# Kernel optimization log

Measured on AMD Instinct MI355X. Metric: run time of the kernel, lower is better.

The kernel has to match this reference:

```python
import jax, jax.numpy as jnp
import numpy as np

B, D, H, E, K = 16384, 1024, 256, 8, 2
EPS = 1e-9


def setup_inputs() -> dict:
    key = jax.random.key(0)
    ks = jax.random.split(key, 4)
    scale_in = 1.0 / np.sqrt(D)
    scale_h = 1.0 / np.sqrt(H)
    return {
        "x": jax.random.normal(ks[0], (B, D), dtype=jnp.float32),
        "gate_w": jax.random.normal(ks[1], (D, E), dtype=jnp.float32) * scale_in,
        "gate_b": jnp.zeros((E,), dtype=jnp.float32),
        "w1": jax.random.normal(ks[2], (E, D, H), dtype=jnp.float32) * scale_in,
        "b1": jnp.zeros((E, H), dtype=jnp.float32),
        "w2": jax.random.normal(ks[3], (E, H, D), dtype=jnp.float32) * scale_h,
        "b2": jnp.zeros((E, D), dtype=jnp.float32),
    }


def reference(x, gate_w, gate_b, w1, b1, w2, b2):
    # Gating: logits -> softmax -> top-k mask -> renormalize (top_k_gating)
    logits = x @ gate_w + gate_b                      # [B, E]
    probs = jax.nn.softmax(logits, axis=-1)           # [B, E]
    _, topk_idx = jax.lax.top_k(probs, K)             # [B, K]
    rows = jnp.arange(probs.shape[0])[:, None]
    mask = jnp.zeros_like(probs).at[rows, topk_idx].set(1.0)
    masked = probs * mask
    denom = jnp.clip(jnp.sum(masked, axis=-1, keepdims=True), EPS, None)
    gating_weights = masked / denom                   # [B, E]

    # Dense all-experts MLP: Linear -> GELU(exact) -> Linear, batched over E
    h = jax.nn.gelu(jnp.einsum('bd,edh->beh', x, w1) + b1, approximate=False)  # [B, E, H]
    expert_outs = jnp.einsum('beh,ehd->bed', h, w2) + b2                        # [B, E, D]

    # Gating-weighted sum over experts
    output = jnp.einsum('bed,be->bd', expert_outs, gating_weights)              # [B, D]
    return output
```

## Files before the change

kernel.cpp:

```cpp
#include <hip/hip_runtime.h>
#include <stdint.h>

#define BN 16384
#define DD 1024
#define HH 256
#define EE 8
#define GB 512
#define GR 32

typedef __attribute__((ext_vector_type(8))) short short8;
typedef __attribute__((ext_vector_type(4))) float floatx4;

__device__ __forceinline__ unsigned short f2bf(float f) {
  union { float f; unsigned int i; } v; v.f = f;
  unsigned int x = v.i;
  x += 0x7fffu + ((x >> 16) & 1u);
  return (unsigned short)(x >> 16);
}
__device__ __forceinline__ unsigned int pack2(float a, float b) {
  return (unsigned int)f2bf(a) | ((unsigned int)f2bf(b) << 16);
}
__device__ __forceinline__ float bf2f(unsigned int u16) {
  union { unsigned int i; float f; } v; v.i = u16 << 16; return v.f;
}
__device__ __forceinline__ void async16(const unsigned short* g, unsigned short* l) {
  __builtin_amdgcn_global_load_lds(
      (const __attribute__((address_space(1))) void*)g,
      (__attribute__((address_space(3))) void*)l, 16, 0, 0);
}

__global__ __launch_bounds__(256) void gating_kernel(
    const float* __restrict__ x,
    const float* __restrict__ gate_w,
    const float* __restrict__ gate_b,
    int* __restrict__ rinfo_e, float* __restrict__ rinfo_w,
    int* __restrict__ bhist,
    unsigned short* __restrict__ xb) {
  __shared__ int hist[EE];
  int tid = threadIdx.x;
  if (tid < EE) hist[tid] = 0;
  __syncthreads();
  int lane = tid & 63, wv = tid >> 6;
#pragma unroll 1
  for (int it = 0; it < GR / 4; it++) {
    int row = blockIdx.x * GR + it * 4 + wv;
    const float4* xr4 = (const float4*)(x + (size_t)row * DD);
    float acc[EE];
#pragma unroll
    for (int e = 0; e < EE; e++) acc[e] = 0.f;
#pragma unroll
    for (int i = 0; i < 4; i++) {
      int d4 = lane + i * 64;
      float4 xv = xr4[d4];
      if (xb) {
        uint2 st; st.x = pack2(xv.x, xv.y); st.y = pack2(xv.z, xv.w);
        *(uint2*)(xb + (size_t)row * DD + (size_t)d4 * 4) = st;
      }
      const float4* gp = (const float4*)gate_w + (size_t)d4 * 8;
      float xs[4] = {xv.x, xv.y, xv.z, xv.w};
#pragma unroll
      for (int j = 0; j < 4; j++) {
        float4 glo = gp[2 * j], ghi = gp[2 * j + 1];
        acc[0] += xs[j] * glo.x; acc[1] += xs[j] * glo.y;
        acc[2] += xs[j] * glo.z; acc[3] += xs[j] * glo.w;
        acc[4] += xs[j] * ghi.x; acc[5] += xs[j] * ghi.y;
        acc[6] += xs[j] * ghi.z; acc[7] += xs[j] * ghi.w;
      }
    }
#pragma unroll
    for (int s = 1; s < 64; s <<= 1) {
#pragma unroll
      for (int e = 0; e < EE; e++) acc[e] += __shfl_xor(acc[e], s, 64);
    }
    if (lane == 0) {
      float lg[EE];
#pragma unroll
      for (int e = 0; e < EE; e++) lg[e] = acc[e] + gate_b[e];
      int i1 = 0;
      for (int e = 1; e < EE; e++) if (lg[e] > lg[i1]) i1 = e;
      int i2 = (i1 == 0) ? 1 : 0;
      for (int e = 0; e < EE; e++) if (e != i1 && lg[e] > lg[i2]) i2 = e;
      float wA = 1.f / (1.f + __expf(lg[i2] - lg[i1]));
      float wB = 1.f - wA;
      rinfo_e[row] = i1 | (i2 << 8);
      rinfo_w[row * 2 + 0] = wA;
      rinfo_w[row * 2 + 1] = wB;
      atomicAdd(&hist[i1], 1);
      atomicAdd(&hist[i2], 1);
    }
  }
  __syncthreads();
  if (tid < EE) bhist[blockIdx.x * EE + tid] = hist[tid];
}

__global__ __launch_bounds__(256) void scan_kernel(
    const int* __restrict__ bhist, int* __restrict__ cnt, int* __restrict__ bbase) {
  __shared__ int cs[32][EE];
  __shared__ int ofs[EE];
  int tid = threadIdx.x;
  int g = tid & 7, c = tid >> 3;
  int s = 0;
#pragma unroll 1
  for (int b = c * 16; b < c * 16 + 16; b++) s += bhist[b * EE + g];
  cs[c][g] = s;
  __syncthreads();
  if (tid == 0) {
    int run = 0;
    for (int gg = 0; gg < EE; gg++) {
      int tot = 0;
      for (int cc = 0; cc < 32; cc++) tot += cs[cc][gg];
      cnt[gg] = tot;
      cnt[32 + gg] = run;
      ofs[gg] = run;
      run += tot;
    }
  }
  __syncthreads();
  if (tid < EE) {
    int run = ofs[tid];
#pragma unroll 1
    for (int cc = 0; cc < 32; cc++) { int t = cs[cc][tid]; cs[cc][tid] = run; run += t; }
  }
  __syncthreads();
  int run = cs[c][g];
#pragma unroll 1
  for (int b = c * 16; b < c * 16 + 16; b++) {
    bbase[b * EE + g] = run;
    run += bhist[b * EE + g];
  }
}

__global__ __launch_bounds__(64) void scatter_kernel(
    const int* __restrict__ rinfo_e, const float* rinfo_w,
    const int* __restrict__ bbase,
    int* __restrict__ rowidx, float* __restrict__ wgt, int* posmap) {
  __shared__ int curs[EE];
  int tid = threadIdx.x;
  if (tid < EE) curs[tid] = bbase[blockIdx.x * EE + tid];
  __syncthreads();
  if (tid < GR) {
    int row = blockIdx.x * GR + tid;
    int ee = rinfo_e[row];
    int e0 = ee & 255, e1 = (ee >> 8) & 255;
    float w0 = rinfo_w[row * 2 + 0];
    float w1 = rinfo_w[row * 2 + 1];
    int p0 = atomicAdd(&curs[e0], 1);
    rowidx[p0] = row; wgt[p0] = w0;
    int p1 = atomicAdd(&curs[e1], 1);
    rowidx[p1] = row; wgt[p1] = w1;
    posmap[row * 2 + 0] = p0;
    posmap[row * 2 + 1] = p1;
  }
}

__global__ void transpose_kernel(const float* __restrict__ src,
                                 unsigned short* __restrict__ dst, int R, int C) {
  __shared__ float tbuf[32][33];
  int e = blockIdx.z;
  int c0 = blockIdx.x * 32, r0 = blockIdx.y * 32;
  int tx = threadIdx.x, ty = threadIdx.y;
  const float* s = src + (size_t)e * R * C;
  unsigned short* d = dst + (size_t)e * R * C;
  for (int yy = ty; yy < 32; yy += 8)
    tbuf[yy][tx] = s[(size_t)(r0 + yy) * C + c0 + tx];
  __syncthreads();
  for (int yy = ty; yy < 32; yy += 8)
    d[(size_t)(c0 + yy) * R + r0 + tx] = f2bf(tbuf[tx][yy]);
}

template <bool ASYNC_A>
__global__ __launch_bounds__(256) void gemm1_kernel(
    const unsigned short* __restrict__ xb,
    const float* __restrict__ x,
    const unsigned short* __restrict__ w1t,
    const float* __restrict__ b1,
    const int* __restrict__ cnt,
    const int* __restrict__ rowidx,
    unsigned short* __restrict__ hbuf,
    int g0, int g1) {
  __shared__ unsigned short As[2][8192];
  __shared__ unsigned short Bs[2][8192];
  int t = blockIdx.x, g = -1, lt = 0;
#pragma unroll 1
  for (int gg = g0; gg < g1; gg++) {
    int nt = (cnt[gg] + 127) >> 7;
    if (t < nt) { g = gg; lt = t; break; }
    t -= nt;
  }
  if (g < 0) return;
  const int* offs = cnt + 32;
  int hb = offs[g0];
  int m0 = offs[g] + lt * 128;
  int mEnd = offs[g] + cnt[g];
  int e = g;
  int n0 = blockIdx.y * 128;
  const unsigned short* Bsrc = w1t + (size_t)e * HH * DD + (size_t)n0 * DD;
  int tid = threadIdx.x, lane = tid & 63, wv = tid >> 6;
  int wr = (wv >> 1) * 64, wc = (wv & 1) * 64;
  int lm = lane & 15, q = lane >> 4;
  int lm7 = lm & 7;
  floatx4 acc[4][4];
  floatx4 zero = {0.f, 0.f, 0.f, 0.f};
#pragma unroll
  for (int i = 0; i < 4; i++)
#pragma unroll
    for (int j = 0; j < 4; j++) acc[i][j] = zero;
  int srow = tid >> 3;
  int ssrc = (((tid & 7) ^ (srow & 7))) * 8;
  int sdst = (tid & 7) * 8;
  const unsigned short* gA[4];
  const float* gAf[4];
  const unsigned short* gBp[4];
#pragma unroll
  for (int i = 0; i < 4; i++) {
    int pos = m0 + i * 32 + srow;
    int grow = rowidx[pos < mEnd ? pos : m0];
    if (ASYNC_A) gA[i] = xb + (size_t)grow * DD + ssrc;
    else         gAf[i] = x + (size_t)grow * DD + ssrc;
    gBp[i] = Bsrc + (size_t)(i * 32 + srow) * DD + ssrc;
  }
  auto stageAsync = [&](int bufi) {
#pragma unroll
    for (int i = 0; i < 4; i++) async16(gA[i], &As[bufi][wv * 512 + i * 2048]);
#pragma unroll
    for (int i = 0; i < 4; i++) gA[i] += 64;
#pragma unroll
    for (int i = 0; i < 4; i++) async16(gBp[i], &Bs[bufi][wv * 512 + i * 2048]);
#pragma unroll
    for (int i = 0; i < 4; i++) gBp[i] += 64;
  };
  auto compute = [&](int bufi) {
#pragma unroll
    for (int ks = 0; ks < 2; ks++) {
      short8 a[4], b[4];
#pragma unroll
      for (int i = 0; i < 4; i++)
        a[i] = *(const short8*)&As[bufi][(wr + i * 16 + lm) * 64 + ((ks * 4 + q) ^ lm7) * 8];
#pragma unroll
      for (int j = 0; j < 4; j++)
        b[j] = *(const short8*)&Bs[bufi][(wc + j * 16 + lm) * 64 + ((ks * 4 + q) ^ lm7) * 8];
#pragma unroll
      for (int i = 0; i < 4; i++)
#pragma unroll
        for (int j = 0; j < 4; j++)
          acc[i][j] = __builtin_amdgcn_mfma_f32_16x16x32_bf16(b[j], a[i], acc[i][j], 0, 0, 0);
    }
  };
  if (ASYNC_A) {
    stageAsync(0);
    __syncthreads();
    int buf = 0;
#pragma unroll 1
    for (int tt = 0; tt < DD / 64; ++tt) {
      if (tt < DD / 64 - 1) stageAsync(buf ^ 1);
      compute(buf);
      __syncthreads();
      buf ^= 1;
    }
  } else {
#pragma unroll 1
    for (int k0 = 0; k0 < DD; k0 += 64) {
#pragma unroll
      for (int i = 0; i < 4; i++) {
        float4 f0 = *(const float4*)gAf[i];
        float4 f1 = *(const float4*)(gAf[i] + 4);
        gAf[i] += 64;
        uint4 av;
        av.x = pack2(f0.x, f0.y); av.y = pack2(f0.z, f0.w);
        av.z = pack2(f1.x, f1.y); av.w = pack2(f1.z, f1.w);
        *(uint4*)&As[0][(i * 32 + srow) * 64 + sdst] = av;
      }
#pragma unroll
      for (int i = 0; i < 4; i++) async16(gBp[i], &Bs[0][wv * 512 + i * 2048]);
#pragma unroll
      for (int i = 0; i < 4; i++) gBp[i] += 64;
      __syncthreads();
      compute(0);
      __syncthreads();
    }
  }
#pragma unroll
  for (int i = 0; i < 4; i++) {
    int pos = m0 + wr + i * 16 + lm;
    if (pos < mEnd) {
#pragma unroll
      for (int j = 0; j < 4; j++) {
        int col = n0 + wc + j * 16 + q * 4;
        const float4 bb = *(const float4*)(b1 + e * HH + col);
        float v0 = acc[i][j][0] + bb.x;
        float v1 = acc[i][j][1] + bb.y;
        float v2 = acc[i][j][2] + bb.z;
        float v3 = acc[i][j][3] + bb.w;
        v0 = 0.5f * v0 * (1.f + erff(v0 * 0.70710678118654752f));
        v1 = 0.5f * v1 * (1.f + erff(v1 * 0.70710678118654752f));
        v2 = 0.5f * v2 * (1.f + erff(v2 * 0.70710678118654752f));
        v3 = 0.5f * v3 * (1.f + erff(v3 * 0.70710678118654752f));
        uint2 st; st.x = pack2(v0, v1); st.y = pack2(v2, v3);
        *(uint2*)(hbuf + (size_t)(pos - hb) * HH + col) = st;
      }
    }
  }
}

template <bool EO>
__global__ __launch_bounds__(256) void gemm2_kernel(
    const unsigned short* __restrict__ hbuf,
    const unsigned short* __restrict__ w2t,
    const float* __restrict__ b2,
    const int* __restrict__ cnt,
    const int* __restrict__ rowidx,
    const float* __restrict__ wgt,
    unsigned short* __restrict__ eo,
    float* out,
    int g0, int g1) {
  __shared__ unsigned short As[128 * 64];
  __shared__ unsigned short Bs[128 * 64];
  int t = blockIdx.x, g = -1, lt = 0;
#pragma unroll 1
  for (int gg = g0; gg < g1; gg++) {
    int nt = (cnt[gg] + 127) >> 7;
    if (t < nt) { g = gg; lt = t; break; }
    t -= nt;
  }
  if (g < 0) return;
  const int* offs = cnt + 32;
  int hb = offs[g0];
  int m0 = offs[g] + lt * 128;
  int mEnd = offs[g] + cnt[g];
  int e = g;
  int n0 = blockIdx.y * 128;
  const unsigned short* Bsrc = w2t + (size_t)e * DD * HH + (size_t)n0 * HH;
  int tid = threadIdx.x, lane = tid & 63, wv = tid >> 6;
  int wr = (wv >> 1) * 64, wc = (wv & 1) * 64;
  int lm = lane & 15, q = lane >> 4;
  int lm7 = lm & 7;
  floatx4 acc[4][4];
  floatx4 zero = {0.f, 0.f, 0.f, 0.f};
#pragma unroll
  for (int i = 0; i < 4; i++)
#pragma unroll
    for (int j = 0; j < 4; j++) acc[i][j] = zero;
  int srow = tid >> 3;
  int ssrc = (((tid & 7) ^ (srow & 7))) * 8;
  const unsigned short* gA[4];
  const unsigned short* gBp[4];
#pragma unroll
  for (int i = 0; i < 4; i++) {
    int pos = m0 + i * 32 + srow;
    int posc = (pos < mEnd) ? pos : m0;
    gA[i] = hbuf + (size_t)(posc - hb) * HH + ssrc;
    gBp[i] = Bsrc + (size_t)(i * 32 + srow) * HH + ssrc;
  }
  unsigned short* AsW = As + wv * 512;
  unsigned short* BsW = Bs + wv * 512;
#pragma unroll 1
  for (int k0 = 0; k0 < HH; k0 += 64) {
#pragma unroll
    for (int i = 0; i < 4; i++) async16(gA[i], AsW + i * 2048);
#pragma unroll
    for (int i = 0; i < 4; i++) async16(gBp[i], BsW + i * 2048);
#pragma unroll
    for (int i = 0; i < 4; i++) { gA[i] += 64; gBp[i] += 64; }
    __syncthreads();
#pragma unroll
    for (int ks = 0; ks < 2; ks++) {
      short8 a[4], b[4];
#pragma unroll
      for (int i = 0; i < 4; i++)
        a[i] = *(const short8*)&As[(wr + i * 16 + lm) * 64 + ((ks * 4 + q) ^ lm7) * 8];
#pragma unroll
      for (int j = 0; j < 4; j++)
        b[j] = *(const short8*)&Bs[(wc + j * 16 + lm) * 64 + ((ks * 4 + q) ^ lm7) * 8];
#pragma unroll
      for (int i = 0; i < 4; i++)
#pragma unroll
        for (int j = 0; j < 4; j++)
          acc[i][j] = __builtin_amdgcn_mfma_f32_16x16x32_bf16(b[j], a[i], acc[i][j], 0, 0, 0);
    }
    __syncthreads();
  }
#pragma unroll
  for (int i = 0; i < 4; i++) {
    int pos = m0 + wr + i * 16 + lm;
    if (pos < mEnd) {
      float wrow = wgt[pos];
      if (EO) {
#pragma unroll
        for (int j = 0; j < 4; j++) {
          int col = n0 + wc + j * 16 + q * 4;
          const float4 bb = *(const float4*)(b2 + e * DD + col);
          uint2 st;
          st.x = pack2((acc[i][j][0] + bb.x) * wrow, (acc[i][j][1] + bb.y) * wrow);
          st.y = pack2((acc[i][j][2] + bb.z) * wrow, (acc[i][j][3] + bb.w) * wrow);
          *(uint2*)(eo + (size_t)pos * DD + col) = st;
        }
      } else {
        int grow = rowidx[pos];
#pragma unroll
        for (int j = 0; j < 4; j++) {
          int col = n0 + wc + j * 16 + q * 4;
          const float4 bb = *(const float4*)(b2 + e * DD + col);
          float* op = out + (size_t)grow * DD + col;
          atomicAdd(op + 0, (acc[i][j][0] + bb.x) * wrow);
          atomicAdd(op + 1, (acc[i][j][1] + bb.y) * wrow);
          atomicAdd(op + 2, (acc[i][j][2] + bb.z) * wrow);
          atomicAdd(op + 3, (acc[i][j][3] + bb.w) * wrow);
        }
      }
    }
  }
}

__global__ __launch_bounds__(256) void combine_kernel(
    const unsigned short* __restrict__ eo, const int* __restrict__ posmap,
    float* __restrict__ out) {
  int row = blockIdx.x * 2 + (threadIdx.x >> 7);
  int t = threadIdx.x & 127;
  int p0 = posmap[row * 2 + 0];
  int p1 = posmap[row * 2 + 1];
  uint4 av = *((const uint4*)(eo + (size_t)p0 * DD) + t);
  uint4 bv = *((const uint4*)(eo + (size_t)p1 * DD) + t);
  unsigned int ua[4] = {av.x, av.y, av.z, av.w};
  unsigned int ub[4] = {bv.x, bv.y, bv.z, bv.w};
  float o[8];
#pragma unroll
  for (int k = 0; k < 4; k++) {
    o[2 * k]     = bf2f(ua[k] & 0xffffu) + bf2f(ub[k] & 0xffffu);
    o[2 * k + 1] = bf2f(ua[k] >> 16)     + bf2f(ub[k] >> 16);
  }
  float* op = out + (size_t)row * DD + t * 8;
  *(float4*)(op)     = make_float4(o[0], o[1], o[2], o[3]);
  *(float4*)(op + 4) = make_float4(o[4], o[5], o[6], o[7]);
}

extern "C" void kernel_launch(void* const* d_in, const int* in_sizes, int n_in,
                              void* d_out, int out_size, void* d_ws, size_t ws_size,
                              hipStream_t stream) {
  (void)in_sizes; (void)n_in; (void)out_size;
  const float* x      = (const float*)d_in[0];
  const float* gate_w = (const float*)d_in[1];
  const float* gate_b = (const float*)d_in[2];
  const float* w1     = (const float*)d_in[3];
  const float* b1     = (const float*)d_in[4];
  const float* w2     = (const float*)d_in[5];
  const float* b2     = (const float*)d_in[6];
  float* out = (float*)d_out;

  char* w = (char*)d_ws;
  int* cnt            = (int*)(w);
  int* rinfo_e        = (int*)(w + 256);
  float* rinfo_w      = (float*)(w + 65792);
  int* posmap         = (int*)(w + 65792);
  int* bhist          = (int*)(w + 196864);
  int* bbase          = (int*)(w + 229632);
  int* rowidx         = (int*)(w + 262400);
  float* wgt          = (float*)(w + 393472);
  unsigned short* w1t = (unsigned short*)(w + 524544);
  unsigned short* w2t = (unsigned short*)(w + 4718848);
  unsigned short* hbuf= (unsigned short*)(w + 8913152);
  unsigned short* xb  = (unsigned short*)(w + 25690368);
  unsigned short* eo  = (unsigned short*)(w + 59244800);
  bool use_xb = ws_size >= (size_t)59244800;
  bool use_eo = ws_size >= (size_t)126353664;

  transpose_kernel<<<dim3(HH / 32, DD / 32, EE), dim3(32, 8), 0, stream>>>(w1, w1t, DD, HH);
  transpose_kernel<<<dim3(DD / 32, HH / 32, EE), dim3(32, 8), 0, stream>>>(w2, w2t, HH, DD);
  gating_kernel<<<GB, 256, 0, stream>>>(x, gate_w, gate_b, rinfo_e, rinfo_w, bhist,
                                        use_xb ? xb : (unsigned short*)nullptr);
  scan_kernel<<<1, 256, 0, stream>>>(bhist, cnt, bbase);
  scatter_kernel<<<GB, 64, 0, stream>>>(rinfo_e, rinfo_w, bbase, rowidx, wgt, posmap);
  if (use_eo) {
    gemm1_kernel<true><<<dim3(264, 2), 256, 0, stream>>>(xb, x, w1t, b1, cnt, rowidx, hbuf, 0, 8);
    gemm2_kernel<true><<<dim3(264, 8), 256, 0, stream>>>(hbuf, w2t, b2, cnt, rowidx, wgt, eo, nullptr, 0, 8);
    combine_kernel<<<BN / 2, 256, 0, stream>>>(eo, posmap, out);
  } else if (use_xb) {
    hipMemsetAsync(out, 0, (size_t)BN * DD * 4, stream);
    gemm1_kernel<true><<<dim3(264, 2), 256, 0, stream>>>(xb, x, w1t, b1, cnt, rowidx, hbuf, 0, 8);
    gemm2_kernel<false><<<dim3(264, 8), 256, 0, stream>>>(hbuf, w2t, b2, cnt, rowidx, wgt, nullptr, out, 0, 8);
  } else {
    hipMemsetAsync(out, 0, (size_t)BN * DD * 4, stream);
    gemm1_kernel<false><<<dim3(264, 2), 256, 0, stream>>>(nullptr, x, w1t, b1, cnt, rowidx, hbuf, 0, 8);
    gemm2_kernel<false><<<dim3(264, 8), 256, 0, stream>>>(hbuf, w2t, b2, cnt, rowidx, wgt, nullptr, out, 0, 8);
  }
}
```

Measured before the change: 298.5 us.

## Shrink gemm1 tile to 128x64, single-buffer LDS, double grid columns

Changes the first expert GEMM from a 128x128 tile with double-buffered async LDS staging to a 128x64 tile with a single LDS buffer and two barriers per k-step. The grid's column dimension doubles from 2 to 4 so the same output is covered. Each wave now owns a 32x64 strip. The aim is lower LDS and register use, allowing more resident blocks and more blocks overall for occupancy. In exchange, the prefetch/compute overlap is gone and each gathered A tile is loaded twice as often.

```diff
diff --git a/kernel.cpp b/kernel.cpp
--- a/kernel.cpp
+++ b/kernel.cpp
@@ -178,8 +178,8 @@
     const int* __restrict__ rowidx,
     unsigned short* __restrict__ hbuf,
     int g0, int g1) {
-  __shared__ unsigned short As[2][8192];
-  __shared__ unsigned short Bs[2][8192];
+  __shared__ unsigned short As[128 * 64];
+  __shared__ unsigned short Bs[64 * 64];
   int t = blockIdx.x, g = -1, lt = 0;
 #pragma unroll 1
   for (int gg = g0; gg < g1; gg++) {
@@ -193,16 +193,16 @@
   int m0 = offs[g] + lt * 128;
   int mEnd = offs[g] + cnt[g];
   int e = g;
-  int n0 = blockIdx.y * 128;
+  int n0 = blockIdx.y * 64;
   const unsigned short* Bsrc = w1t + (size_t)e * HH * DD + (size_t)n0 * DD;
   int tid = threadIdx.x, lane = tid & 63, wv = tid >> 6;
-  int wr = (wv >> 1) * 64, wc = (wv & 1) * 64;
+  int wr = wv * 32;
   int lm = lane & 15, q = lane >> 4;
   int lm7 = lm & 7;
-  floatx4 acc[4][4];
+  floatx4 acc[2][4];
   floatx4 zero = {0.f, 0.f, 0.f, 0.f};
 #pragma unroll
-  for (int i = 0; i < 4; i++)
+  for (int i = 0; i < 2; i++)
 #pragma unroll
     for (int j = 0; j < 4; j++) acc[i][j] = zero;
   int srow = tid >> 3;
@@ -210,56 +210,25 @@
   int sdst = (tid & 7) * 8;
   const unsigned short* gA[4];
   const float* gAf[4];
-  const unsigned short* gBp[4];
+  const unsigned short* gBp[2];
 #pragma unroll
   for (int i = 0; i < 4; i++) {
     int pos = m0 + i * 32 + srow;
     int grow = rowidx[pos < mEnd ? pos : m0];
     if (ASYNC_A) gA[i] = xb + (size_t)grow * DD + ssrc;
     else         gAf[i] = x + (size_t)grow * DD + ssrc;
+  }
+#pragma unroll
+  for (int i = 0; i < 2; i++)
     gBp[i] = Bsrc + (size_t)(i * 32 + srow) * DD + ssrc;
-  }
-  auto stageAsync = [&](int bufi) {
-#pragma unroll
-    for (int i = 0; i < 4; i++) async16(gA[i], &As[bufi][wv * 512 + i * 2048]);
-#pragma unroll
-    for (int i = 0; i < 4; i++) gA[i] += 64;
-#pragma unroll
-    for (int i = 0; i < 4; i++) async16(gBp[i], &Bs[bufi][wv * 512 + i * 2048]);
-#pragma unroll
-    for (int i = 0; i < 4; i++) gBp[i] += 64;
-  };
-  auto compute = [&](int bufi) {
-#pragma unroll
-    for (int ks = 0; ks < 2; ks++) {
-      short8 a[4], b[4];
-#pragma unroll
-      for (int i = 0; i < 4; i++)
-        a[i] = *(const short8*)&As[bufi][(wr + i * 16 + lm) * 64 + ((ks * 4 + q) ^ lm7) * 8];
-#pragma unroll
-      for (int j = 0; j < 4; j++)
-        b[j] = *(const short8*)&Bs[bufi][(wc + j * 16 + lm) * 64 + ((ks * 4 + q) ^ lm7) * 8];
-#pragma unroll
-      for (int i = 0; i < 4; i++)
-#pragma unroll
-        for (int j = 0; j < 4; j++)
-          acc[i][j] = __builtin_amdgcn_mfma_f32_16x16x32_bf16(b[j], a[i], acc[i][j], 0, 0, 0);
-    }
-  };
-  if (ASYNC_A) {
-    stageAsync(0);
-    __syncthreads();
-    int buf = 0;
-#pragma unroll 1
-    for (int tt = 0; tt < DD / 64; ++tt) {
-      if (tt < DD / 64 - 1) stageAsync(buf ^ 1);
-      compute(buf);
-      __syncthreads();
-      buf ^= 1;
-    }
-  } else {
-#pragma unroll 1
-    for (int k0 = 0; k0 < DD; k0 += 64) {
+#pragma unroll 1
+  for (int k0 = 0; k0 < DD; k0 += 64) {
+    if (ASYNC_A) {
+#pragma unroll
+      for (int i = 0; i < 4; i++) async16(gA[i], &As[wv * 512 + i * 2048]);
+#pragma unroll
+      for (int i = 0; i < 4; i++) gA[i] += 64;
+    } else {
 #pragma unroll
       for (int i = 0; i < 4; i++) {
         float4 f0 = *(const float4*)gAf[i];
@@ -268,24 +237,38 @@
         uint4 av;
         av.x = pack2(f0.x, f0.y); av.y = pack2(f0.z, f0.w);
         av.z = pack2(f1.x, f1.y); av.w = pack2(f1.z, f1.w);
-        *(uint4*)&As[0][(i * 32 + srow) * 64 + sdst] = av;
+        *(uint4*)&As[(i * 32 + srow) * 64 + sdst] = av;
       }
-#pragma unroll
-      for (int i = 0; i < 4; i++) async16(gBp[i], &Bs[0][wv * 512 + i * 2048]);
-#pragma unroll
-      for (int i = 0; i < 4; i++) gBp[i] += 64;
-      __syncthreads();
-      compute(0);
-      __syncthreads();
-    }
-  }
-#pragma unroll
-  for (int i = 0; i < 4; i++) {
+    }
+#pragma unroll
+    for (int i = 0; i < 2; i++) async16(gBp[i], &Bs[wv * 512 + i * 2048]);
+#pragma unroll
+    for (int i = 0; i < 2; i++) gBp[i] += 64;
+    __syncthreads();
+#pragma unroll
+    for (int ks = 0; ks < 2; ks++) {
+      short8 a[2], b[4];
+#pragma unroll
+      for (int i = 0; i < 2; i++)
+        a[i] = *(const short8*)&As[(wr + i * 16 + lm) * 64 + ((ks * 4 + q) ^ lm7) * 8];
+#pragma unroll
+      for (int j = 0; j < 4; j++)
+        b[j] = *(const short8*)&Bs[(j * 16 + lm) * 64 + ((ks * 4 + q) ^ lm7) * 8];
+#pragma unroll
+      for (int i = 0; i < 2; i++)
+#pragma unroll
+        for (int j = 0; j < 4; j++)
+          acc[i][j] = __builtin_amdgcn_mfma_f32_16x16x32_bf16(b[j], a[i], acc[i][j], 0, 0, 0);
+    }
+    __syncthreads();
+  }
+#pragma unroll
+  for (int i = 0; i < 2; i++) {
     int pos = m0 + wr + i * 16 + lm;
     if (pos < mEnd) {
 #pragma unroll
       for (int j = 0; j < 4; j++) {
-        int col = n0 + wc + j * 16 + q * 4;
+        int col = n0 + j * 16 + q * 4;
         const float4 bb = *(const float4*)(b1 + e * HH + col);
         float v0 = acc[i][j][0] + bb.x;
         float v1 = acc[i][j][1] + bb.y;
@@ -470,16 +453,16 @@
   scan_kernel<<<1, 256, 0, stream>>>(bhist, cnt, bbase);
   scatter_kernel<<<GB, 64, 0, stream>>>(rinfo_e, rinfo_w, bbase, rowidx, wgt, posmap);
   if (use_eo) {
-    gemm1_kernel<true><<<dim3(264, 2), 256, 0, stream>>>(xb, x, w1t, b1, cnt, rowidx, hbuf, 0, 8);
+    gemm1_kernel<true><<<dim3(264, 4), 256, 0, stream>>>(xb, x, w1t, b1, cnt, rowidx, hbuf, 0, 8);
     gemm2_kernel<true><<<dim3(264, 8), 256, 0, stream>>>(hbuf, w2t, b2, cnt, rowidx, wgt, eo, nullptr, 0, 8);
     combine_kernel<<<BN / 2, 256, 0, stream>>>(eo, posmap, out);
   } else if (use_xb) {
     hipMemsetAsync(out, 0, (size_t)BN * DD * 4, stream);
-    gemm1_kernel<true><<<dim3(264, 2), 256, 0, stream>>>(xb, x, w1t, b1, cnt, rowidx, hbuf, 0, 8);
+    gemm1_kernel<true><<<dim3(264, 4), 256, 0, stream>>>(xb, x, w1t, b1, cnt, rowidx, hbuf, 0, 8);
     gemm2_kernel<false><<<dim3(264, 8), 256, 0, stream>>>(hbuf, w2t, b2, cnt, rowidx, wgt, nullptr, out, 0, 8);
   } else {
     hipMemsetAsync(out, 0, (size_t)BN * DD * 4, stream);
-    gemm1_kernel<false><<<dim3(264, 2), 256, 0, stream>>>(nullptr, x, w1t, b1, cnt, rowidx, hbuf, 0, 8);
+    gemm1_kernel<false><<<dim3(264, 4), 256, 0, stream>>>(nullptr, x, w1t, b1, cnt, rowidx, hbuf, 0, 8);
     gemm2_kernel<false><<<dim3(264, 8), 256, 0, stream>>>(hbuf, w2t, b2, cnt, rowidx, wgt, nullptr, out, 0, 8);
   }
 }
```

Result: faster. 286.4 us (-4.1%).
